# Optimization experiments

Measured on AMD Instinct MI355X. Metric: run time of the kernel, lower is better.

## Reference

```python
import jax, jax.numpy as jnp
import numpy as np

L, H, P = 32768, 256, 256
DT_MIN, DT_MAX = 0.001, 0.1


def setup_inputs() -> dict:
    key = jax.random.key(0)
    ks = jax.random.split(key, 7)
    signal = jax.random.normal(ks[0], (L, H), jnp.float32)
    # stable HiPPO-like init: negative real part, random imaginary part
    lam_re = -(0.1 + 0.4 * jax.random.uniform(ks[1], (P,), jnp.float32))
    lam_im = jax.random.normal(ks[2], (P,), jnp.float32)
    Lambda_ri = jnp.stack([lam_re, lam_im], axis=-1)            # (P, 2)
    B_ri = jax.random.normal(ks[3], (P, H, 2), jnp.float32) / np.float32(np.sqrt(H))
    C_ri = jax.random.normal(ks[4], (H, P, 2), jnp.float32) / np.float32(np.sqrt(P))
    D = jax.random.uniform(ks[5], (H,), jnp.float32)
    log_step = jnp.log(DT_MIN + (DT_MAX - DT_MIN) * jax.random.uniform(ks[6], (P,), jnp.float32))
    return {"signal": signal, "Lambda_ri": Lambda_ri, "B_ri": B_ri,
            "C_ri": C_ri, "D": D, "log_step": log_step}


def reference(signal, Lambda_ri, B_ri, C_ri, D, log_step):
    # --- get_BC_tilde (bcInit='dense'): B stored real (P,H,2) -> complex ---
    Lambda = jax.lax.complex(Lambda_ri[..., 0], Lambda_ri[..., 1])   # (P,)
    B_tilde = jax.lax.complex(B_ri[..., 0], B_ri[..., 1])            # (P, H)
    C_tilde = jax.lax.complex(C_ri[..., 0], C_ri[..., 1])            # (H, P)

    # --- discretize_zoh ---
    step = jnp.exp(log_step)                                          # (P,) step_scale = 1.0
    Lambda_bar = jnp.exp(Lambda * step)                               # (P,) complex
    B_bar = ((Lambda_bar - 1.0) / Lambda)[:, None] * B_tilde          # (P, H) complex

    # --- apply_ssm: Bu_elements = vmap(u -> B_bar @ u) over time ---
    Bu = signal.astype(Lambda_bar.dtype) @ B_bar.T                    # (L, P) complex
    Lam = jnp.broadcast_to(Lambda_bar, Bu.shape)                      # (L, P)

    def binop(qi, qj):
        A_i, Bu_i = qi
        A_j, Bu_j = qj
        return (A_j * A_i, Bu_j + A_j * Bu_i)

    _, xs = jax.lax.associative_scan(binop, (Lam, Bu), axis=0)        # (L, P)

    # y = Re(C_tilde @ x) + D * u, vectorized over time
    y = jnp.real(xs @ C_tilde.T) + D * signal                         # (L, H)
    return y
```

## Files before the change

### kernel.cpp

```cpp
#include <hip/hip_runtime.h>
#include <math.h>

constexpr int L = 32768;
constexpr int H = 256;
constexpr int P = 256;
constexpr int T = 64;
constexpr int NC = L / T;
constexpr int N1 = 2 * P;
constexpr int LDA = 40;
constexpr int LDEP = 130;

typedef __attribute__((ext_vector_type(8))) short short8;
typedef __attribute__((ext_vector_type(4))) float f32x4;

__device__ __forceinline__ unsigned f2bf(float f) {
  unsigned u = __float_as_uint(f);
  return (u + 0x7FFFu + ((u >> 16) & 1u)) >> 16;
}
__device__ __forceinline__ float bf_lo(unsigned u) { return __uint_as_float(u << 16); }
__device__ __forceinline__ float bf_hi(unsigned u) { return __uint_as_float(u & 0xFFFF0000u); }

__device__ __forceinline__ void gload_lds16(const unsigned short* g, unsigned short* l) {
  __builtin_amdgcn_global_load_lds(
      (const __attribute__((address_space(1))) unsigned int*)(g),
      (__attribute__((address_space(3))) unsigned int*)(l), 16, 0, 0);
}

__device__ __forceinline__ void lambda_bar_of(const float* __restrict__ lam,
                                              const float* __restrict__ lstep,
                                              int p, float& lbr, float& lbi) {
  float lr = lam[2 * p], li = lam[2 * p + 1];
  float st = expf(lstep[p]);
  float ea = expf(lr * st);
  lbr = ea * cosf(li * st);
  lbi = ea * sinf(li * st);
}

__global__ __launch_bounds__(256) void k_prep(const float* __restrict__ lam,
                                              const float* __restrict__ lstep,
                                              const float* __restrict__ Bri,
                                              const float* __restrict__ Cri,
                                              unsigned short* __restrict__ Bcat,
                                              unsigned short* __restrict__ Ccat,
                                              float* __restrict__ powr,
                                              float* __restrict__ powi) {
  int idx = blockIdx.x * 256 + threadIdx.x;
  if (idx < N1 * H) {
    int n = idx >> 8, k = idx & 255;
    int p = n >> 1, comp = n & 1;
    float lr = lam[2 * p], li = lam[2 * p + 1];
    float st = expf(lstep[p]);
    float ea = expf(lr * st);
    float lbr = ea * cosf(li * st), lbi = ea * sinf(li * st);
    float inv = 1.0f / (lr * lr + li * li);
    float nr = lbr - 1.0f;
    float fr = (nr * lr + lbi * li) * inv;
    float fi = (lbi * lr - nr * li) * inv;
    float br = Bri[2 * (p * H + k)], bi = Bri[2 * (p * H + k) + 1];
    float v = (comp == 0) ? (fr * br - fi * bi) : (fr * bi + fi * br);
    Bcat[idx] = (unsigned short)f2bf(v);
  } else if (idx < 2 * N1 * H) {
    int j = idx - N1 * H;
    int h = j >> 9, k2 = j & 511;
    int p = k2 >> 1;
    float v = ((k2 & 1) == 0) ? Cri[2 * (h * P + p)] : -Cri[2 * (h * P + p) + 1];
    Ccat[j] = (unsigned short)f2bf(v);
  } else {
    int r = idx - 2 * N1 * H;
    int t = r >> 8, p = r & 255;
    float lr = lam[2 * p], li = lam[2 * p + 1];
    float st = expf(lstep[p]);
    float e = (float)(t + 1);
    float er = expf(e * lr * st);
    powr[r] = er * cosf(e * li * st);
    powi[r] = er * sinf(e * li * st);
  }
}

__global__ __launch_bounds__(256) void k_gemm1s(const float* __restrict__ sig,
                                                const unsigned short* __restrict__ Bcat,
                                                const float* __restrict__ lam,
                                                const float* __restrict__ lstep,
                                                unsigned short* __restrict__ Xl,
                                                float* __restrict__ Sr,
                                                float* __restrict__ Si) {
  constexpr int K = 256, NIT = K / 32;
  __shared__ __align__(16) char smem[36864];
  unsigned short* sA[2] = {(unsigned short*)smem, (unsigned short*)smem + 5120};
  unsigned short* sB[2] = {(unsigned short*)smem + 10240, (unsigned short*)smem + 14336};
  float* sEpi = (float*)smem;
  const int tid = threadIdx.x;
  const int lane = tid & 63;
  const int wave = tid >> 6;
  const int wr = (wave >> 1) * 64, wc = (wave & 1) * 64;
  const int m0 = blockIdx.x * 128, n0 = blockIdx.y * 128;
  const int ar = tid >> 1, aq = (tid & 1) * 16;
  const int br = tid >> 2, bq = (tid & 3) * 8;
  const int frow = lane & 15, fk = (lane >> 4) * 8;
  f32x4 acc[4][4];
#pragma unroll
  for (int i = 0; i < 4; i++)
#pragma unroll
    for (int j = 0; j < 4; j++) acc[i][j] = (f32x4){0.f, 0.f, 0.f, 0.f};

  float4 aR[4];
  const float* abase = sig + (size_t)(m0 + ar) * K + aq;
#define LOAD_A(k0) { const float* s_ = abase + (k0); \
    aR[0] = *(const float4*)(s_); aR[1] = *(const float4*)(s_ + 4); \
    aR[2] = *(const float4*)(s_ + 8); aR[3] = *(const float4*)(s_ + 12); }
#define WRITE_A(buf) { uint4 w0, w1; \
    w0.x = f2bf(aR[0].x) | (f2bf(aR[0].y) << 16); w0.y = f2bf(aR[0].z) | (f2bf(aR[0].w) << 16); \
    w0.z = f2bf(aR[1].x) | (f2bf(aR[1].y) << 16); w0.w = f2bf(aR[1].z) | (f2bf(aR[1].w) << 16); \
    w1.x = f2bf(aR[2].x) | (f2bf(aR[2].y) << 16); w1.y = f2bf(aR[2].z) | (f2bf(aR[2].w) << 16); \
    w1.z = f2bf(aR[3].x) | (f2bf(aR[3].y) << 16); w1.w = f2bf(aR[3].z) | (f2bf(aR[3].w) << 16); \
    *(uint4*)(sA[buf] + ar * LDA + aq) = w0; *(uint4*)(sA[buf] + ar * LDA + aq + 8) = w1; }
#define ISSUE_B(k0, buf) { \
    gload_lds16(Bcat + (size_t)(n0 + br) * K + (k0) + bq, sB[buf] + tid * 8); \
    gload_lds16(Bcat + (size_t)(n0 + 64 + br) * K + (k0) + bq, sB[buf] + 2048 + tid * 8); }

  LOAD_A(0);
  ISSUE_B(0, 0);
  WRITE_A(0);
  LOAD_A(32);
  __syncthreads();
#pragma unroll
  for (int it = 0; it < NIT; it++) {
    const int cur = it & 1, nxt = cur ^ 1;
    if (it + 1 < NIT) {
      WRITE_A(nxt);
      ISSUE_B((it + 1) * 32, nxt);
      if (it + 2 < NIT) LOAD_A((it + 2) * 32);
    }
    short8 af[4], bf[4];
#pragma unroll
    for (int i = 0; i < 4; i++) af[i] = *(const short8*)(sA[cur] + (wr + i * 16 + frow) * LDA + fk);
#pragma unroll
    for (int j = 0; j < 4; j++) bf[j] = *(const short8*)(sB[cur] + (wc + j * 16 + frow) * 32 + fk);
#pragma unroll
    for (int i = 0; i < 4; i++)
#pragma unroll
      for (int j = 0; j < 4; j++)
        acc[i][j] = __builtin_amdgcn_mfma_f32_16x16x32_bf16(af[i], bf[j], acc[i][j], 0, 0, 0);
    __syncthreads();
  }

  const int crow = (lane >> 4) * 4, ccol = wc + (lane & 15);
#pragma unroll
  for (int half = 0; half < 2; half++) {
    if ((wave >> 1) == half) {
#pragma unroll
      for (int i = 0; i < 4; i++)
#pragma unroll
        for (int j = 0; j < 4; j++)
#pragma unroll
          for (int g = 0; g < 4; g++)
            sEpi[(crow + i * 16 + g) * LDEP + ccol + j * 16] = acc[i][j][g];
    }
    __syncthreads();
    if (tid < 64) {
      const int pl = tid;
      const int gp = (n0 >> 1) + pl;
      const int c = blockIdx.x * 2 + half;
      float lbr, lbi;
      lambda_bar_of(lam, lstep, gp, lbr, lbi);
      float xr = 0.f, xi = 0.f;
      const float* e = sEpi + 2 * pl;
      const size_t gbase = (size_t)(m0 + half * 64) * N1 + n0 + 2 * pl;
      for (int tb = 0; tb < T; tb += 8) {
        float2 v[8];
#pragma unroll
        for (int u = 0; u < 8; u++) v[u] = *(const float2*)(e + (tb + u) * LDEP);
        unsigned ov[8];
#pragma unroll
        for (int u = 0; u < 8; u++) {
          float nr = fmaf(lbr, xr, fmaf(-lbi, xi, v[u].x));
          float ni = fmaf(lbr, xi, fmaf(lbi, xr, v[u].y));
          xr = nr; xi = ni;
          ov[u] = f2bf(xr) | (f2bf(xi) << 16);
        }
#pragma unroll
        for (int u = 0; u < 8; u++)
          *(unsigned*)(Xl + gbase + (size_t)(tb + u) * N1) = ov[u];
      }
      Sr[c * P + gp] = xr;
      Si[c * P + gp] = xi;
    }
    __syncthreads();
  }
#undef LOAD_A
#undef WRITE_A
#undef ISSUE_B
}

__global__ __launch_bounds__(64) void k_carry2(const float* __restrict__ lam,
                                               const float* __restrict__ lstep,
                                               const float* __restrict__ Sr,
                                               const float* __restrict__ Si,
                                               float* __restrict__ car, float* __restrict__ cai) {
  const int p = blockIdx.x;
  const int t = threadIdx.x;
  float lr = lam[2 * p], li = lam[2 * p + 1];
  float st = expf(lstep[p]);
  float eT = expf((float)T * lr * st);
  float lTr = eT * cosf((float)T * li * st);
  float lTi = eT * sinf((float)T * li * st);
  float vr[8], vi[8];
#pragma unroll
  for (int u = 0; u < 8; u++) {
    vr[u] = Sr[(t * 8 + u) * P + p];
    vi[u] = Si[(t * 8 + u) * P + p];
  }
  float Br = 0.f, Bi = 0.f;
#pragma unroll
  for (int u = 0; u < 8; u++) {
    float nr = fmaf(lTr, Br, fmaf(-lTi, Bi, vr[u]));
    float ni = fmaf(lTr, Bi, fmaf(lTi, Br, vi[u]));
    Br = nr; Bi = ni;
  }
  float e8 = expf(8.0f * (float)T * lr * st);
  float Ar = e8 * cosf(8.0f * (float)T * li * st);
  float Ai = e8 * sinf(8.0f * (float)T * li * st);
#pragma unroll
  for (int d = 1; d < 64; d <<= 1) {
    float Aor = __shfl_up(Ar, d), Aoi = __shfl_up(Ai, d);
    float Bor = __shfl_up(Br, d), Boi = __shfl_up(Bi, d);
    if (t >= d) {
      float nBr = Ar * Bor - Ai * Boi + Br;
      float nBi = Ar * Boi + Ai * Bor + Bi;
      float nAr = Aor * Ar - Aoi * Ai;
      float nAi = Aor * Ai + Aoi * Ar;
      Br = nBr; Bi = nBi; Ar = nAr; Ai = nAi;
    }
  }
  float cr = __shfl_up(Br, 1), ci = __shfl_up(Bi, 1);
  if (t == 0) { cr = 0.f; ci = 0.f; }
#pragma unroll
  for (int u = 0; u < 8; u++) {
    car[(t * 8 + u) * P + p] = cr;
    cai[(t * 8 + u) * P + p] = ci;
    float nr = fmaf(lTr, cr, fmaf(-lTi, ci, vr[u]));
    float ni = fmaf(lTr, ci, fmaf(lTi, cr, vi[u]));
    cr = nr; ci = ni;
  }
}

__global__ __launch_bounds__(256) void k_gemm2f(const unsigned short* __restrict__ Xl,
                                                const unsigned short* __restrict__ Ccat,
                                                const float* __restrict__ powr,
                                                const float* __restrict__ powi,
                                                const float* __restrict__ car,
                                                const float* __restrict__ cai,
                                                const float* __restrict__ sig,
                                                const float* __restrict__ Dv,
                                                float* __restrict__ out) {
  constexpr int K = 512, NIT = K / 32;
  __shared__ __align__(16) char smem[36864];
  unsigned short* sA[2] = {(unsigned short*)smem, (unsigned short*)smem + 5120};
  unsigned short* sB[2] = {(unsigned short*)smem + 10240, (unsigned short*)smem + 14336};
  const int tid = threadIdx.x;
  const int lane = tid & 63;
  const int wave = tid >> 6;
  const int wr = (wave >> 1) * 64, wc = (wave & 1) * 64;
  const int m0 = blockIdx.x * 128, n0 = blockIdx.y * 128;
  const int ar = tid >> 1, aq = (tid & 1) * 16;
  const int t_ = ar & 63;
  const int cc = blockIdx.x * 2 + (ar >> 6);
  const int br = tid >> 2, bq = (tid & 3) * 8;
  const int frow = lane & 15, fk = (lane >> 4) * 8;
  f32x4 acc[4][4];
#pragma unroll
  for (int i = 0; i < 4; i++)
#pragma unroll
    for (int j = 0; j < 4; j++) acc[i][j] = (f32x4){0.f, 0.f, 0.f, 0.f};

  uint4 x0, x1;
  float4 pr0, pr1, pi0, pi1, cr0, cr1, ci0, ci1;
  const unsigned short* xbase = Xl + (size_t)(m0 + ar) * N1 + aq;
  const float* prb = powr + t_ * P;
  const float* pib = powi + t_ * P;
  const float* crb = car + cc * P;
  const float* cib = cai + cc * P;
#define LOAD_A2(k0) { int p0_ = ((k0) >> 1) + (tid & 1) * 8; \
    x0 = *(const uint4*)(xbase + (k0)); x1 = *(const uint4*)(xbase + (k0) + 8); \
    pr0 = *(const float4*)(prb + p0_); pr1 = *(const float4*)(prb + p0_ + 4); \
    pi0 = *(const float4*)(pib + p0_); pi1 = *(const float4*)(pib + p0_ + 4); \
    cr0 = *(const float4*)(crb + p0_); cr1 = *(const float4*)(crb + p0_ + 4); \
    ci0 = *(const float4*)(cib + p0_); ci1 = *(const float4*)(cib + p0_ + 4); }
#define WRITE_A2(buf) { \
    unsigned xw[8] = {x0.x, x0.y, x0.z, x0.w, x1.x, x1.y, x1.z, x1.w}; \
    float pr_[8] = {pr0.x, pr0.y, pr0.z, pr0.w, pr1.x, pr1.y, pr1.z, pr1.w}; \
    float pi_[8] = {pi0.x, pi0.y, pi0.z, pi0.w, pi1.x, pi1.y, pi1.z, pi1.w}; \
    float cr_[8] = {cr0.x, cr0.y, cr0.z, cr0.w, cr1.x, cr1.y, cr1.z, cr1.w}; \
    float ci_[8] = {ci0.x, ci0.y, ci0.z, ci0.w, ci1.x, ci1.y, ci1.z, ci1.w}; \
    unsigned wo[8]; \
    _Pragma("unroll") for (int j_ = 0; j_ < 8; j_++) { \
      float xgr = bf_lo(xw[j_]) + (pr_[j_] * cr_[j_] - pi_[j_] * ci_[j_]); \
      float xgi = bf_hi(xw[j_]) + (pr_[j_] * ci_[j_] + pi_[j_] * cr_[j_]); \
      wo[j_] = f2bf(xgr) | (f2bf(xgi) << 16); } \
    uint4 w0, w1; \
    w0.x = wo[0]; w0.y = wo[1]; w0.z = wo[2]; w0.w = wo[3]; \
    w1.x = wo[4]; w1.y = wo[5]; w1.z = wo[6]; w1.w = wo[7]; \
    *(uint4*)(sA[buf] + ar * LDA + aq) = w0; *(uint4*)(sA[buf] + ar * LDA + aq + 8) = w1; }
#define ISSUE_B2(k0, buf) { \
    gload_lds16(Ccat + (size_t)(n0 + br) * K + (k0) + bq, sB[buf] + tid * 8); \
    gload_lds16(Ccat + (size_t)(n0 + 64 + br) * K + (k0) + bq, sB[buf] + 2048 + tid * 8); }

  LOAD_A2(0);
  ISSUE_B2(0, 0);
  WRITE_A2(0);
  LOAD_A2(32);
  __syncthreads();
#pragma unroll
  for (int it = 0; it < NIT; it++) {
    const int cur = it & 1, nxt = cur ^ 1;
    if (it + 1 < NIT) {
      WRITE_A2(nxt);
      ISSUE_B2((it + 1) * 32, nxt);
      if (it + 2 < NIT) LOAD_A2((it + 2) * 32);
    }
    short8 af[4], bf[4];
#pragma unroll
    for (int i = 0; i < 4; i++) af[i] = *(const short8*)(sA[cur] + (wr + i * 16 + frow) * LDA + fk);
#pragma unroll
    for (int j = 0; j < 4; j++) bf[j] = *(const short8*)(sB[cur] + (wc + j * 16 + frow) * 32 + fk);
#pragma unroll
    for (int i = 0; i < 4; i++)
#pragma unroll
      for (int j = 0; j < 4; j++)
        acc[i][j] = __builtin_amdgcn_mfma_f32_16x16x32_bf16(af[i], bf[j], acc[i][j], 0, 0, 0);
    __syncthreads();
  }

  const int crow = wr + (lane >> 4) * 4, ccol = wc + (lane & 15);
  float dcol[4];
#pragma unroll
  for (int j = 0; j < 4; j++) dcol[j] = Dv[n0 + ccol + j * 16];
#pragma unroll
  for (int i = 0; i < 4; i++)
#pragma unroll
    for (int j = 0; j < 4; j++) {
      int col = n0 + ccol + j * 16;
#pragma unroll
      for (int g = 0; g < 4; g++) {
        int row = m0 + crow + i * 16 + g;
        out[(size_t)row * H + col] = acc[i][j][g] + dcol[j] * sig[(size_t)row * H + col];
      }
    }
#undef LOAD_A2
#undef WRITE_A2
#undef ISSUE_B2
}

extern "C" void kernel_launch(void* const* d_in, const int* in_sizes, int n_in,
                              void* d_out, int out_size, void* d_ws, size_t ws_size,
                              hipStream_t stream) {
  const float* sig = (const float*)d_in[0];
  const float* lam = (const float*)d_in[1];
  const float* Bri = (const float*)d_in[2];
  const float* Cri = (const float*)d_in[3];
  const float* Dv  = (const float*)d_in[4];
  const float* lst = (const float*)d_in[5];
  float* out = (float*)d_out;

  unsigned short* Bcat = (unsigned short*)d_ws;
  unsigned short* Ccat = Bcat + (size_t)N1 * H;
  unsigned short* Xl   = Ccat + (size_t)H * N1;
  float* powr = (float*)(Xl + (size_t)L * N1);
  float* powi = powr + T * P;
  float* Sr   = powi + T * P;
  float* Si   = Sr + NC * P;
  float* car  = Si + NC * P;
  float* cai  = car + NC * P;

  k_prep<<<(2 * N1 * H + T * P) / 256, 256, 0, stream>>>(lam, lst, Bri, Cri,
                                                         Bcat, Ccat, powr, powi);
  dim3 g1(L / 128, N1 / 128);
  k_gemm1s<<<g1, 256, 0, stream>>>(sig, Bcat, lam, lst, Xl, Sr, Si);
  k_carry2<<<NC / 2, 64, 0, stream>>>(lam, lst, Sr, Si, car, cai);
  dim3 g2(L / 128, H / 128);
  k_gemm2f<<<g2, 256, 0, stream>>>(Xl, Ccat, powr, powi, car, cai, sig, Dv, out);
}
```

Measured before the change: 154.7 us.

## Deepen GEMM prefetch pipeline with explicit vmcnt barriers and fragment-ordered B layout

Both GEMM kernels now keep two register stages of A-operand global loads in flight, so A prefetch runs three iterations ahead. The generic __syncthreads is replaced by a custom barrier that waits only on the older vector-memory ops via partial vmcnt counts, with sched_barrier fences pinning the load order. The B tile is loaded into LDS in MFMA fragment order so each wave reads contiguous 16-byte chunks, and gemm1 gets a launch-bounds occupancy hint. The hand-counted vmcnt values are fragile: if the compiler emits a different number of memory ops, this risks races or extra stalls, and the extra registers may reduce occupancy.

```diff
diff --git a/kernel.cpp b/kernel.cpp
--- a/kernel.cpp
+++ b/kernel.cpp
@@ -25,6 +25,14 @@
       (const __attribute__((address_space(1))) unsigned int*)(g),
       (__attribute__((address_space(3))) unsigned int*)(l), 16, 0, 0);
 }
+
+#define KBAR(N) do { \
+    asm volatile("s_waitcnt vmcnt(" #N ") lgkmcnt(0)" ::: "memory"); \
+    __builtin_amdgcn_s_barrier(); \
+    __builtin_amdgcn_sched_barrier(0); \
+  } while (0)
+
+#define VMEM_FENCE() __builtin_amdgcn_sched_barrier(0x38F)
 
 __device__ __forceinline__ void lambda_bar_of(const float* __restrict__ lam,
                                               const float* __restrict__ lstep,
@@ -77,13 +85,13 @@
   }
 }
 
-__global__ __launch_bounds__(256) void k_gemm1s(const float* __restrict__ sig,
-                                                const unsigned short* __restrict__ Bcat,
-                                                const float* __restrict__ lam,
-                                                const float* __restrict__ lstep,
-                                                unsigned short* __restrict__ Xl,
-                                                float* __restrict__ Sr,
-                                                float* __restrict__ Si) {
+__global__ __launch_bounds__(256, 4) void k_gemm1s(const float* __restrict__ sig,
+                                                   const unsigned short* __restrict__ Bcat,
+                                                   const float* __restrict__ lam,
+                                                   const float* __restrict__ lstep,
+                                                   unsigned short* __restrict__ Xl,
+                                                   float* __restrict__ Sr,
+                                                   float* __restrict__ Si) {
   constexpr int K = 256, NIT = K / 32;
   __shared__ __align__(16) char smem[36864];
   unsigned short* sA[2] = {(unsigned short*)smem, (unsigned short*)smem + 5120};
@@ -95,54 +103,65 @@
   const int wr = (wave >> 1) * 64, wc = (wave & 1) * 64;
   const int m0 = blockIdx.x * 128, n0 = blockIdx.y * 128;
   const int ar = tid >> 1, aq = (tid & 1) * 16;
-  const int br = tid >> 2, bq = (tid & 3) * 8;
+  const int brow = ((tid >> 6) << 4) | (tid & 15);
+  const int bko = ((tid >> 4) & 3) * 8;
   const int frow = lane & 15, fk = (lane >> 4) * 8;
+  const int hb = (wave & 1) * 2048;
   f32x4 acc[4][4];
 #pragma unroll
   for (int i = 0; i < 4; i++)
 #pragma unroll
     for (int j = 0; j < 4; j++) acc[i][j] = (f32x4){0.f, 0.f, 0.f, 0.f};
 
-  float4 aR[4];
+  float4 aR0[4], aR1[4];
   const float* abase = sig + (size_t)(m0 + ar) * K + aq;
-#define LOAD_A(k0) { const float* s_ = abase + (k0); \
-    aR[0] = *(const float4*)(s_); aR[1] = *(const float4*)(s_ + 4); \
-    aR[2] = *(const float4*)(s_ + 8); aR[3] = *(const float4*)(s_ + 12); }
-#define WRITE_A(buf) { uint4 w0, w1; \
-    w0.x = f2bf(aR[0].x) | (f2bf(aR[0].y) << 16); w0.y = f2bf(aR[0].z) | (f2bf(aR[0].w) << 16); \
-    w0.z = f2bf(aR[1].x) | (f2bf(aR[1].y) << 16); w0.w = f2bf(aR[1].z) | (f2bf(aR[1].w) << 16); \
-    w1.x = f2bf(aR[2].x) | (f2bf(aR[2].y) << 16); w1.y = f2bf(aR[2].z) | (f2bf(aR[2].w) << 16); \
-    w1.z = f2bf(aR[3].x) | (f2bf(aR[3].y) << 16); w1.w = f2bf(aR[3].z) | (f2bf(aR[3].w) << 16); \
-    *(uint4*)(sA[buf] + ar * LDA + aq) = w0; *(uint4*)(sA[buf] + ar * LDA + aq + 8) = w1; }
+#define LOAD_A(R, k0) { const float* s_ = abase + (k0); \
+    R[0] = *(const float4*)(s_); R[1] = *(const float4*)(s_ + 4); \
+    R[2] = *(const float4*)(s_ + 8); R[3] = *(const float4*)(s_ + 12); }
+#define WRITE_A(R, dst) { uint4 w0, w1; \
+    w0.x = f2bf(R[0].x) | (f2bf(R[0].y) << 16); w0.y = f2bf(R[0].z) | (f2bf(R[0].w) << 16); \
+    w0.z = f2bf(R[1].x) | (f2bf(R[1].y) << 16); w0.w = f2bf(R[1].z) | (f2bf(R[1].w) << 16); \
+    w1.x = f2bf(R[2].x) | (f2bf(R[2].y) << 16); w1.y = f2bf(R[2].z) | (f2bf(R[2].w) << 16); \
+    w1.z = f2bf(R[3].x) | (f2bf(R[3].y) << 16); w1.w = f2bf(R[3].z) | (f2bf(R[3].w) << 16); \
+    *(uint4*)((dst) + ar * LDA + aq) = w0; *(uint4*)((dst) + ar * LDA + aq + 8) = w1; }
 #define ISSUE_B(k0, buf) { \
-    gload_lds16(Bcat + (size_t)(n0 + br) * K + (k0) + bq, sB[buf] + tid * 8); \
-    gload_lds16(Bcat + (size_t)(n0 + 64 + br) * K + (k0) + bq, sB[buf] + 2048 + tid * 8); }
-
-  LOAD_A(0);
+    gload_lds16(Bcat + (size_t)(n0 + brow) * K + (k0) + bko, sB[buf] + tid * 8); \
+    gload_lds16(Bcat + (size_t)(n0 + 64 + brow) * K + (k0) + bko, sB[buf] + 2048 + tid * 8); }
+
+  LOAD_A(aR0, 0);
+  LOAD_A(aR1, 32);
+  VMEM_FENCE();
   ISSUE_B(0, 0);
-  WRITE_A(0);
-  LOAD_A(32);
-  __syncthreads();
+  VMEM_FENCE();
+  WRITE_A(aR0, sA[0]);
+  LOAD_A(aR0, 64);
+  KBAR(4);
 #pragma unroll
   for (int it = 0; it < NIT; it++) {
     const int cur = it & 1, nxt = cur ^ 1;
     if (it + 1 < NIT) {
-      WRITE_A(nxt);
+      if (((it + 1) & 1) == 0) { WRITE_A(aR0, sA[nxt]); } else { WRITE_A(aR1, sA[nxt]); }
       ISSUE_B((it + 1) * 32, nxt);
-      if (it + 2 < NIT) LOAD_A((it + 2) * 32);
-    }
-    short8 af[4], bf[4];
+    }
+    VMEM_FENCE();
+    if (it + 3 < NIT) {
+      if (((it + 3) & 1) == 0) { LOAD_A(aR0, (it + 3) * 32); } else { LOAD_A(aR1, (it + 3) * 32); }
+    }
+    short8 af[4], bfr[4];
 #pragma unroll
     for (int i = 0; i < 4; i++) af[i] = *(const short8*)(sA[cur] + (wr + i * 16 + frow) * LDA + fk);
 #pragma unroll
-    for (int j = 0; j < 4; j++) bf[j] = *(const short8*)(sB[cur] + (wc + j * 16 + frow) * 32 + fk);
+    for (int j = 0; j < 4; j++) bfr[j] = *(const short8*)(sB[cur] + hb + (j * 64 + lane) * 8);
 #pragma unroll
     for (int i = 0; i < 4; i++)
 #pragma unroll
       for (int j = 0; j < 4; j++)
-        acc[i][j] = __builtin_amdgcn_mfma_f32_16x16x32_bf16(af[i], bf[j], acc[i][j], 0, 0, 0);
-    __syncthreads();
-  }
+        acc[i][j] = __builtin_amdgcn_mfma_f32_16x16x32_bf16(af[i], bfr[j], acc[i][j], 0, 0, 0);
+    if (it + 1 < NIT) {
+      if (it + 3 < NIT) { KBAR(4); } else { KBAR(0); }
+    }
+  }
+  __syncthreads();
 
   const int crow = (lane >> 4) * 4, ccol = wc + (lane & 15);
 #pragma unroll
@@ -265,29 +284,32 @@
   const int ar = tid >> 1, aq = (tid & 1) * 16;
   const int t_ = ar & 63;
   const int cc = blockIdx.x * 2 + (ar >> 6);
-  const int br = tid >> 2, bq = (tid & 3) * 8;
+  const int brow = ((tid >> 6) << 4) | (tid & 15);
+  const int bko = ((tid >> 4) & 3) * 8;
   const int frow = lane & 15, fk = (lane >> 4) * 8;
+  const int hb = (wave & 1) * 2048;
   f32x4 acc[4][4];
 #pragma unroll
   for (int i = 0; i < 4; i++)
 #pragma unroll
     for (int j = 0; j < 4; j++) acc[i][j] = (f32x4){0.f, 0.f, 0.f, 0.f};
 
-  uint4 x0, x1;
+  uint4 x0a, x1a, x0b, x1b;
   float4 pr0, pr1, pi0, pi1, cr0, cr1, ci0, ci1;
   const unsigned short* xbase = Xl + (size_t)(m0 + ar) * N1 + aq;
   const float* prb = powr + t_ * P;
   const float* pib = powi + t_ * P;
   const float* crb = car + cc * P;
   const float* cib = cai + cc * P;
-#define LOAD_A2(k0) { int p0_ = ((k0) >> 1) + (tid & 1) * 8; \
-    x0 = *(const uint4*)(xbase + (k0)); x1 = *(const uint4*)(xbase + (k0) + 8); \
+#define LOAD_X(A0, A1, k0) { \
+    A0 = *(const uint4*)(xbase + (k0)); A1 = *(const uint4*)(xbase + (k0) + 8); }
+#define LOAD_PC(k0) { const int p0_ = ((k0) >> 1) + (tid & 1) * 8; \
     pr0 = *(const float4*)(prb + p0_); pr1 = *(const float4*)(prb + p0_ + 4); \
     pi0 = *(const float4*)(pib + p0_); pi1 = *(const float4*)(pib + p0_ + 4); \
     cr0 = *(const float4*)(crb + p0_); cr1 = *(const float4*)(crb + p0_ + 4); \
     ci0 = *(const float4*)(cib + p0_); ci1 = *(const float4*)(cib + p0_ + 4); }
-#define WRITE_A2(buf) { \
-    unsigned xw[8] = {x0.x, x0.y, x0.z, x0.w, x1.x, x1.y, x1.z, x1.w}; \
+#define WRITE_A2(XA, XB, dst) { \
+    unsigned xw[8] = {XA.x, XA.y, XA.z, XA.w, XB.x, XB.y, XB.z, XB.w}; \
     float pr_[8] = {pr0.x, pr0.y, pr0.z, pr0.w, pr1.x, pr1.y, pr1.z, pr1.w}; \
     float pi_[8] = {pi0.x, pi0.y, pi0.z, pi0.w, pi1.x, pi1.y, pi1.z, pi1.w}; \
     float cr_[8] = {cr0.x, cr0.y, cr0.z, cr0.w, cr1.x, cr1.y, cr1.z, cr1.w}; \
@@ -300,35 +322,48 @@
     uint4 w0, w1; \
     w0.x = wo[0]; w0.y = wo[1]; w0.z = wo[2]; w0.w = wo[3]; \
     w1.x = wo[4]; w1.y = wo[5]; w1.z = wo[6]; w1.w = wo[7]; \
-    *(uint4*)(sA[buf] + ar * LDA + aq) = w0; *(uint4*)(sA[buf] + ar * LDA + aq + 8) = w1; }
+    *(uint4*)((dst) + ar * LDA + aq) = w0; *(uint4*)((dst) + ar * LDA + aq + 8) = w1; }
 #define ISSUE_B2(k0, buf) { \
-    gload_lds16(Ccat + (size_t)(n0 + br) * K + (k0) + bq, sB[buf] + tid * 8); \
-    gload_lds16(Ccat + (size_t)(n0 + 64 + br) * K + (k0) + bq, sB[buf] + 2048 + tid * 8); }
-
-  LOAD_A2(0);
+    gload_lds16(Ccat + (size_t)(n0 + brow) * K + (k0) + bko, sB[buf] + tid * 8); \
+    gload_lds16(Ccat + (size_t)(n0 + 64 + brow) * K + (k0) + bko, sB[buf] + 2048 + tid * 8); }
+
+  LOAD_X(x0a, x1a, 0);
+  LOAD_X(x0b, x1b, 32);
+  LOAD_PC(0);
+  VMEM_FENCE();
   ISSUE_B2(0, 0);
-  WRITE_A2(0);
-  LOAD_A2(32);
-  __syncthreads();
+  VMEM_FENCE();
+  WRITE_A2(x0a, x1a, sA[0]);
+  LOAD_X(x0a, x1a, 64);
+  LOAD_PC(32);
+  KBAR(10);
 #pragma unroll
   for (int it = 0; it < NIT; it++) {
     const int cur = it & 1, nxt = cur ^ 1;
     if (it + 1 < NIT) {
-      WRITE_A2(nxt);
+      if (((it + 1) & 1) == 0) { WRITE_A2(x0a, x1a, sA[nxt]); } else { WRITE_A2(x0b, x1b, sA[nxt]); }
       ISSUE_B2((it + 1) * 32, nxt);
-      if (it + 2 < NIT) LOAD_A2((it + 2) * 32);
-    }
-    short8 af[4], bf[4];
+    }
+    VMEM_FENCE();
+    if (it + 3 < NIT) {
+      if (((it + 3) & 1) == 0) { LOAD_X(x0a, x1a, (it + 3) * 32); } else { LOAD_X(x0b, x1b, (it + 3) * 32); }
+    }
+    if (it + 2 < NIT) LOAD_PC((it + 2) * 32);
+    short8 af[4], bfr[4];
 #pragma unroll
     for (int i = 0; i < 4; i++) af[i] = *(const short8*)(sA[cur] + (wr + i * 16 + frow) * LDA + fk);
 #pragma unroll
-    for (int j = 0; j < 4; j++) bf[j] = *(const short8*)(sB[cur] + (wc + j * 16 + frow) * 32 + fk);
+    for (int j = 0; j < 4; j++) bfr[j] = *(const short8*)(sB[cur] + hb + (j * 64 + lane) * 8);
 #pragma unroll
     for (int i = 0; i < 4; i++)
 #pragma unroll
       for (int j = 0; j < 4; j++)
-        acc[i][j] = __builtin_amdgcn_mfma_f32_16x16x32_bf16(af[i], bf[j], acc[i][j], 0, 0, 0);
-    __syncthreads();
+        acc[i][j] = __builtin_amdgcn_mfma_f32_16x16x32_bf16(af[i], bfr[j], acc[i][j], 0, 0, 0);
+    if (it + 1 < NIT) {
+      if (it + 3 < NIT) { KBAR(10); }
+      else if (it + 2 < NIT) { KBAR(8); }
+      else { KBAR(0); }
+    }
   }
 
   const int crow = wr + (lane >> 4) * 4, ccol = wc + (lane & 15);
@@ -346,7 +381,8 @@
         out[(size_t)row * H + col] = acc[i][j][g] + dcol[j] * sig[(size_t)row * H + col];
       }
     }
-#undef LOAD_A2
+#undef LOAD_X
+#undef LOAD_PC
 #undef WRITE_A2
 #undef ISSUE_B2
 }
```

New measurement: 150.8 us. 1.03x faster.
